# Optimization experiments

Hardware: AMD Instinct MI355X
Metric: run time of the kernel (lower is better)

## Reference

```python
import jax, jax.numpy as jnp
import numpy as np

EMBED_DIM = 1024
NUM_HEADS = 16
HEAD_DIM = EMBED_DIM // NUM_HEADS
EPS = 1e-5


def setup_inputs() -> dict:
    key = jax.random.key(0)
    ks = jax.random.split(key, 7)
    B, S, D = 4, 2048, EMBED_DIM
    s = 1.0 / np.sqrt(D)
    return {
        "x": jax.random.normal(ks[0], (B, S, D), dtype=jnp.float32),
        "W_qkv": jax.random.uniform(ks[1], (D, 3 * D), jnp.float32, -s, s),
        "b_qkv": jax.random.uniform(ks[2], (3 * D,), jnp.float32, -s, s),
        "W_out": jax.random.uniform(ks[3], (D, D), jnp.float32, -s, s),
        "b_out": jax.random.uniform(ks[4], (D,), jnp.float32, -s, s),
        "gamma": jnp.ones((D,), jnp.float32),
        "beta": jnp.zeros((D,), jnp.float32),
    }


def _layer_norm(y, gamma, beta):
    mu = jnp.mean(y, axis=-1, keepdims=True)
    var = jnp.mean(jnp.square(y - mu), axis=-1, keepdims=True)
    return (y - mu) * jax.lax.rsqrt(var + EPS) * gamma + beta


def reference(x, W_qkv, b_qkv, W_out, b_out, gamma, beta):
    B, S, D = x.shape
    H, Hd = NUM_HEADS, HEAD_DIM
    qkv = x @ W_qkv + b_qkv                       # [B,S,3D]
    q, k, v = jnp.split(qkv, 3, axis=-1)
    q = q.reshape(B, S, H, Hd).transpose(0, 2, 1, 3)  # [B,H,S,Hd]
    k = k.reshape(B, S, H, Hd).transpose(0, 2, 1, 3)
    v = v.reshape(B, S, H, Hd).transpose(0, 2, 1, 3)
    scale = 1.0 / np.sqrt(Hd)
    scores = jnp.einsum("bhsd,bhtd->bhst", q, k) * scale  # [B,H,S,S]
    attn = jax.nn.softmax(scores, axis=-1)
    ctx = jnp.einsum("bhst,bhtd->bhsd", attn, v)  # [B,H,S,Hd]
    ctx = ctx.transpose(0, 2, 1, 3).reshape(B, S, D)
    out = ctx @ W_out + b_out
    return _layer_norm(out + x, gamma, beta)
```

## Files before the change

### kernel.cpp

```cpp
#include <hip/hip_runtime.h>
#include <stdint.h>
#include <stddef.h>


#define SEQ    2048
#define DMODEL 1024
#define NHEAD  16
#define HDIM   64

typedef __attribute__((ext_vector_type(4))) float f32x4;
typedef __attribute__((ext_vector_type(16))) float f32x16;
typedef __attribute__((ext_vector_type(8))) short bf16x8;
typedef __attribute__((ext_vector_type(2))) unsigned uint2v;

static __device__ __forceinline__ unsigned short f2b(float f) {
  union { float f; unsigned u; } c; c.f = f;
  unsigned r = c.u + 0x7FFFu + ((c.u >> 16) & 1u);
  return (unsigned short)(r >> 16);
}
static __device__ __forceinline__ unsigned pkbf(float lo, float hi_) {
  unsigned r;
  asm("v_cvt_pk_bf16_f32 %0, %1, %2" : "=v"(r) : "v"(lo), "v"(hi_));
  return r;
}
static __device__ __forceinline__ float exp2v(float x) {
  return __builtin_amdgcn_exp2f(x);
}
static __device__ __forceinline__ uint2v swap32(unsigned a, unsigned b) {
  return __builtin_amdgcn_permlane32_swap(a, b, false, false);
}
static __device__ __forceinline__ float xchg_sum(float v) {
  union { float f; unsigned u; } c; c.f = v;
  uint2v p = swap32(c.u, c.u);
  union { unsigned u; float f; } x, y; x.u = p[0]; y.u = p[1];
  return x.f + y.f;
}
static __device__ __forceinline__ void gl_lds16(const void* g, void* l) {
  __builtin_amdgcn_global_load_lds((const __attribute__((address_space(1))) void*)g,
                                   (__attribute__((address_space(3))) void*)l, 16, 0, 0);
}
static __device__ __forceinline__ int swz(int row, int col) {
  return (row * 64 + col) ^ ((row & 7) << 3);
}

__global__ __launch_bounds__(256) void k_prep(const float* __restrict__ Wqkv,
                                              const float* __restrict__ Wout,
                                              const float* __restrict__ X,
                                              unsigned short* __restrict__ wqkvT,
                                              unsigned short* __restrict__ woutT,
                                              unsigned short* __restrict__ Xb) {
  __shared__ unsigned short tile[32][33];
  const int bid = blockIdx.x;
  const int t = threadIdx.x;
  if (bid < 4096) {
    const float* in; unsigned short* out; int C, bx, by;
    if (bid < 3072) { in = Wqkv; out = wqkvT; C = 3072; bx = bid % 96; by = bid / 96; }
    else { int b2 = bid - 3072; in = Wout; out = woutT; C = 1024; bx = b2 & 31; by = b2 >> 5; }
    const int R = 1024;
    const int c0 = bx * 32, r0 = by * 32;
    const int tx = t & 31, ty = t >> 5;
#pragma unroll
    for (int j = 0; j < 4; j++) {
      int rr = ty + j * 8;
      tile[rr][tx] = f2b(in[(size_t)(r0 + rr) * C + c0 + tx]);
    }
    __syncthreads();
#pragma unroll
    for (int j = 0; j < 4; j++) {
      int rr = ty + j * 8;
      out[(size_t)(c0 + rr) * R + r0 + tx] = tile[tx][rr];
    }
  } else {
    const size_t i = ((size_t)(bid - 4096) * 256 + t) * 8;
    f32x4 a = *(const f32x4*)&X[i];
    f32x4 b = *(const f32x4*)&X[i + 4];
    bf16x8 o;
    o[0] = (short)f2b(a[0]); o[1] = (short)f2b(a[1]);
    o[2] = (short)f2b(a[2]); o[3] = (short)f2b(a[3]);
    o[4] = (short)f2b(b[0]); o[5] = (short)f2b(b[1]);
    o[6] = (short)f2b(b[2]); o[7] = (short)f2b(b[3]);
    *(bf16x8*)&Xb[i] = o;
  }
}

__global__ __launch_bounds__(256) void k_gemm_qkv(const unsigned short* __restrict__ X,
                                                  const unsigned short* __restrict__ WT,
                                                  const float* __restrict__ bias,
                                                  unsigned short* __restrict__ qb,
                                                  unsigned short* __restrict__ kb,
                                                  unsigned short* __restrict__ vt) {
  __shared__ __align__(16) unsigned short As[128 * 32];
  __shared__ __align__(16) unsigned short Bs[128 * 32];
  const int t = threadIdx.x;
  const int w = t >> 6, l = t & 63, g = l >> 4, r = l & 15;
  const int wr = w >> 1, wc = w & 1;
  const int bm = blockIdx.x * 128;
  const int bn = blockIdx.y * 128;

  f32x4 acc[4][4];
#pragma unroll
  for (int a = 0; a < 4; a++)
#pragma unroll
    for (int b = 0; b < 4; b++) acc[a][b] = f32x4{0.f, 0.f, 0.f, 0.f};

  for (int k0 = 0; k0 < DMODEL; k0 += 32) {
    __syncthreads();
#pragma unroll
    for (int j = 0; j < 2; j++) {
      int idx = t + j * 256;
      int row = idx >> 2, kc = idx & 3;
      gl_lds16(X + (size_t)(bm + row) * DMODEL + k0 + kc * 8, (char*)As + idx * 16);
      gl_lds16(WT + (size_t)(bn + row) * DMODEL + k0 + kc * 8, (char*)Bs + idx * 16);
    }
    __syncthreads();
    bf16x8 af[4], bf[4];
#pragma unroll
    for (int mf = 0; mf < 4; mf++)
      af[mf] = *(const bf16x8*)&As[(wr * 64 + mf * 16 + r) * 32 + g * 8];
#pragma unroll
    for (int nf = 0; nf < 4; nf++)
      bf[nf] = *(const bf16x8*)&Bs[(wc * 64 + nf * 16 + r) * 32 + g * 8];
#pragma unroll
    for (int mf = 0; mf < 4; mf++)
#pragma unroll
      for (int nf = 0; nf < 4; nf++)
        acc[mf][nf] = __builtin_amdgcn_mfma_f32_16x16x32_bf16(af[mf], bf[nf], acc[mf][nf], 0, 0, 0);
  }

  if (blockIdx.y >= 16) {
    __syncthreads();
    const int bi = bm >> 11, sbase = bm & 2047;
    const int h  = ((bn - 2048) >> 6) + wc;
    const int bh = bi * NHEAD + h;
    unsigned short* Ls = (w < 2) ? (As + w * 2048) : (Bs + (w - 2) * 2048);
#pragma unroll
    for (int p = 0; p < 2; p++) {
#pragma unroll
      for (int nfp = 0; nfp < 2; nfp++)
#pragma unroll
        for (int mf = 0; mf < 4; mf++)
#pragma unroll
          for (int i = 0; i < 4; i++) {
            const int nf = 2 * p + nfp;
            const int dd = nfp * 16 + r;
            const int ss = mf * 16 + g * 4 + i;
            float v = acc[mf][nf][i] + bias[bn + wc * 64 + nf * 16 + r];
            Ls[dd * 64 + (((ss >> 3) ^ (dd & 7)) * 8) + (ss & 7)] = f2b(v);
          }
#pragma unroll
      for (int j = 0; j < 4; j++) {
        const int dd = l >> 1;
        const int ch = (l & 1) * 4 + j;
        bf16x8 ov = *(const bf16x8*)&Ls[dd * 64 + ((ch ^ (dd & 7)) * 8)];
        *(bf16x8*)&vt[((size_t)bh * HDIM + 32 * p + dd) * SEQ + sbase + wr * 64 + ch * 8] = ov;
      }
    }
  } else {
#pragma unroll
    for (int mf = 0; mf < 4; mf++)
#pragma unroll
      for (int nf = 0; nf < 4; nf++)
#pragma unroll
        for (int i = 0; i < 4; i++) {
          int m = bm + wr * 64 + mf * 16 + g * 4 + i;
          int n = bn + wc * 64 + nf * 16 + r;
          float v = acc[mf][nf][i] + bias[n];
          int part = n >> 10, rem = n & 1023, h = rem >> 6, d = rem & 63;
          int bi = m >> 11, s = m & 2047;
          int bh = bi * NHEAD + h;
          if (part == 0)      qb[((size_t)bh * SEQ + s) * HDIM + d] = f2b(v * 0.18033688f);
          else                kb[((size_t)bh * SEQ + s) * HDIM + d] = f2b(v);
        }
  }
}

__global__ __launch_bounds__(512) void k_attn(const unsigned short* __restrict__ qb,
                                              const unsigned short* __restrict__ kb,
                                              const unsigned short* __restrict__ vt,
                                              unsigned short* __restrict__ ctx) {
  __shared__ __align__(16) unsigned short S[16384];
  unsigned short* K0 = S;
  unsigned short* K1 = S + 4096;
  unsigned short* V0 = S + 8192;
  unsigned short* V1 = S + 12288;
  const int t = threadIdx.x;
  const int w = t >> 6, l = t & 63;
  const int ql = l & 31, hi = l >> 5;
  const int bid = blockIdx.x;
  const int xcd = bid & 7;
  const int j_  = bid >> 3;
  const int bh  = xcd * 8 + (j_ >> 3);
  const int q0  = (j_ & 7) * 256;
  const size_t qoff = ((size_t)bh * SEQ + q0) * HDIM;

#pragma unroll
  for (int j = 0; j < 4; j++) {
    int idx = t + j * 512;
    int row = idx >> 3, s = idx & 7;
    gl_lds16(qb + qoff + (size_t)row * 64 + (s ^ (row & 7)) * 8, (char*)S + idx * 16);
  }
  asm volatile("s_waitcnt vmcnt(0)" ::: "memory");
  __builtin_amdgcn_sched_barrier(0);
  __builtin_amdgcn_s_barrier();

  bf16x8 qf[4];
#pragma unroll
  for (int ds = 0; ds < 4; ds++)
    qf[ds] = *(const bf16x8*)&S[swz(w * 32 + ql, ds * 16 + hi * 8)];
  asm volatile("s_waitcnt lgkmcnt(0)" ::: "memory");
  __builtin_amdgcn_sched_barrier(0);
  __builtin_amdgcn_s_barrier();

  {
    int row = t >> 3, s = t & 7;
    gl_lds16(kb + ((size_t)bh * SEQ + row) * HDIM + (s ^ (row & 7)) * 8, (char*)K0 + t * 16);
    gl_lds16(vt + ((size_t)bh * HDIM + row) * SEQ + (s ^ (row & 7)) * 8, (char*)V0 + t * 16);
  }

  f32x16 acc_o[2];
  float l_run = 0.f;
#pragma unroll
  for (int db = 0; db < 2; db++)
#pragma unroll
    for (int i = 0; i < 16; i++) acc_o[db][i] = 0.f;

  for (int it = 0; it < SEQ / 64; ++it) {
    const int b = it & 1;
    if (it + 1 < SEQ / 64) {
      const int kt = (it + 1) * 64;
      unsigned short* Kd = b ? K0 : K1;
      unsigned short* Vd = b ? V0 : V1;
      {
        int row = t >> 3, s = t & 7;
        gl_lds16(kb + ((size_t)bh * SEQ + kt + row) * HDIM + (s ^ (row & 7)) * 8,
                 (char*)Kd + t * 16);
        gl_lds16(vt + ((size_t)bh * HDIM + row) * SEQ + kt + (s ^ (row & 7)) * 8,
                 (char*)Vd + t * 16);
      }
      asm volatile("s_waitcnt vmcnt(2)" ::: "memory");
    } else {
      asm volatile("s_waitcnt vmcnt(0)" ::: "memory");
    }
    __builtin_amdgcn_sched_barrier(0);
    __builtin_amdgcn_s_barrier();

    const unsigned short* Kb = b ? K1 : K0;
    const unsigned short* Vb = b ? V1 : V0;

    bf16x8 kf[2][4];
#pragma unroll
    for (int kb2 = 0; kb2 < 2; kb2++)
#pragma unroll
      for (int ds = 0; ds < 4; ds++)
        kf[kb2][ds] = *(const bf16x8*)&Kb[swz(kb2 * 32 + ql, ds * 16 + hi * 8)];

    f32x16 accs[2];
#pragma unroll
    for (int kb2 = 0; kb2 < 2; kb2++)
#pragma unroll
      for (int i = 0; i < 16; i++) accs[kb2][i] = 0.f;
    __builtin_amdgcn_s_setprio(1);
#pragma unroll
    for (int ds = 0; ds < 4; ds++)
#pragma unroll
      for (int kb2 = 0; kb2 < 2; kb2++)
        accs[kb2] = __builtin_amdgcn_mfma_f32_32x32x16_bf16(kf[kb2][ds], qf[ds], accs[kb2], 0, 0, 0);
    __builtin_amdgcn_s_setprio(0);

#pragma unroll
    for (int kb2 = 0; kb2 < 2; kb2++)
#pragma unroll
      for (int i = 0; i < 16; i++) accs[kb2][i] = exp2v(accs[kb2][i]);
    float s8[8];
#pragma unroll
    for (int i = 0; i < 8; i++)
      s8[i] = (accs[0][i] + accs[0][i + 8]) + (accs[1][i] + accs[1][i + 8]);
    float sum = ((s8[0] + s8[1]) + (s8[2] + s8[3])) + ((s8[4] + s8[5]) + (s8[6] + s8[7]));
    sum = xchg_sum(sum);
    l_run += sum;

    bf16x8 pa[4];
#pragma unroll
    for (int ks = 0; ks < 4; ks++) {
      const int kb2 = ks >> 1, rb = (ks & 1) * 8;
      unsigned wA0 = pkbf(accs[kb2][rb + 0], accs[kb2][rb + 1]);
      unsigned wA1 = pkbf(accs[kb2][rb + 2], accs[kb2][rb + 3]);
      unsigned wB0 = pkbf(accs[kb2][rb + 4], accs[kb2][rb + 5]);
      unsigned wB1 = pkbf(accs[kb2][rb + 6], accs[kb2][rb + 7]);
      uint2v s0 = swap32(wB0, wA0);
      uint2v s1 = swap32(wB1, wA1);
      union { bf16x8 v; unsigned u[4]; } fr;
      fr.u[0] = s0[1]; fr.u[1] = s1[1]; fr.u[2] = s0[0]; fr.u[3] = s1[0];
      pa[ks] = fr.v;
    }

    bf16x8 vf[2][4];
#pragma unroll
    for (int db = 0; db < 2; db++)
#pragma unroll
      for (int ks = 0; ks < 4; ks++)
        vf[db][ks] = *(const bf16x8*)&Vb[swz(db * 32 + ql, ks * 16 + hi * 8)];

    __builtin_amdgcn_s_setprio(1);
#pragma unroll
    for (int ks = 0; ks < 4; ks++)
#pragma unroll
      for (int db = 0; db < 2; db++)
        acc_o[db] = __builtin_amdgcn_mfma_f32_32x32x16_bf16(vf[db][ks], pa[ks], acc_o[db], 0, 0, 0);
    __builtin_amdgcn_s_setprio(0);

    __builtin_amdgcn_s_barrier();
  }

  const int bi = bh >> 4, h = bh & 15;
  const float rl = 1.f / l_run;
  unsigned short* Ls = S + w * 2048;
#pragma unroll
  for (int db = 0; db < 2; db++)
#pragma unroll
    for (int j = 0; j < 8; j++) {
      const int d0 = db * 32 + (j & 1) * 2 + (j >> 1) * 8 + hi * 4;
      *(unsigned*)&Ls[(ql * 64 + d0) ^ ((ql & 7) << 3)] =
          pkbf(acc_o[db][2 * j] * rl, acc_o[db][2 * j + 1] * rl);
    }
#pragma unroll
  for (int rq = 0; rq < 4; rq++) {
    const int q = rq * 8 + (l >> 3);
    const int c8 = l & 7;
    bf16x8 ov = *(const bf16x8*)&Ls[(q * 64 + c8 * 8) ^ ((q & 7) << 3)];
    *(bf16x8*)&ctx[((size_t)bi * SEQ + q0 + w * 32 + q) * DMODEL + h * 64 + c8 * 8] = ov;
  }
}

__global__ __launch_bounds__(256) void k_gemm_out(const unsigned short* __restrict__ A,
                                                  const unsigned short* __restrict__ WT,
                                                  const float* __restrict__ bias,
                                                  const float* __restrict__ X,
                                                  float* __restrict__ Y) {
  __shared__ __align__(16) unsigned short As[128 * 32];
  __shared__ __align__(16) unsigned short Bs[128 * 32];
  const int t = threadIdx.x;
  const int w = t >> 6, l = t & 63, g = l >> 4, r = l & 15;
  const int wr = w >> 1, wc = w & 1;
  const int bm = blockIdx.x * 128;
  const int bn = blockIdx.y * 128;

  f32x4 acc[4][4];
#pragma unroll
  for (int a = 0; a < 4; a++)
#pragma unroll
    for (int b = 0; b < 4; b++) acc[a][b] = f32x4{0.f, 0.f, 0.f, 0.f};

  for (int k0 = 0; k0 < DMODEL; k0 += 32) {
    __syncthreads();
#pragma unroll
    for (int j = 0; j < 2; j++) {
      int idx = t + j * 256;
      int row = idx >> 2, kc = idx & 3;
      gl_lds16(A + (size_t)(bm + row) * DMODEL + k0 + kc * 8, (char*)As + idx * 16);
      gl_lds16(WT + (size_t)(bn + row) * DMODEL + k0 + kc * 8, (char*)Bs + idx * 16);
    }
    __syncthreads();
    bf16x8 af[4], bf[4];
#pragma unroll
    for (int mf = 0; mf < 4; mf++)
      af[mf] = *(const bf16x8*)&As[(wr * 64 + mf * 16 + r) * 32 + g * 8];
#pragma unroll
    for (int nf = 0; nf < 4; nf++)
      bf[nf] = *(const bf16x8*)&Bs[(wc * 64 + nf * 16 + r) * 32 + g * 8];
#pragma unroll
    for (int mf = 0; mf < 4; mf++)
#pragma unroll
      for (int nf = 0; nf < 4; nf++)
        acc[mf][nf] = __builtin_amdgcn_mfma_f32_16x16x32_bf16(af[mf], bf[nf], acc[mf][nf], 0, 0, 0);
  }

#pragma unroll
  for (int mf = 0; mf < 4; mf++)
#pragma unroll
    for (int nf = 0; nf < 4; nf++)
#pragma unroll
      for (int i = 0; i < 4; i++) {
        int m = bm + wr * 64 + mf * 16 + g * 4 + i;
        int n = bn + wc * 64 + nf * 16 + r;
        float v = acc[mf][nf][i] + bias[n] + X[(size_t)m * DMODEL + n];
        Y[(size_t)m * DMODEL + n] = v;
      }
}

__global__ __launch_bounds__(256) void k_ln(const float* __restrict__ Y,
                                            const float* __restrict__ gamma,
                                            const float* __restrict__ beta,
                                            float* __restrict__ out) {
  const int row = blockIdx.x, t = threadIdx.x;
  const float* y = Y + (size_t)row * DMODEL;
  f32x4 v = *(const f32x4*)&y[t * 4];
  float s = v[0] + v[1] + v[2] + v[3];
  float q = v[0] * v[0] + v[1] * v[1] + v[2] * v[2] + v[3] * v[3];
#pragma unroll
  for (int m = 1; m < 64; m <<= 1) { s += __shfl_xor(s, m); q += __shfl_xor(q, m); }
  __shared__ float ss[4], sq[4];
  const int w = t >> 6, l = t & 63;
  if (l == 0) { ss[w] = s; sq[w] = q; }
  __syncthreads();
  s = ss[0] + ss[1] + ss[2] + ss[3];
  q = sq[0] + sq[1] + sq[2] + sq[3];
  const float mu = s * (1.f / DMODEL);
  const float var = q * (1.f / DMODEL) - mu * mu;
  const float rs = rsqrtf(var + 1e-5f);
  f32x4 o;
#pragma unroll
  for (int j = 0; j < 4; j++)
    o[j] = (v[j] - mu) * rs * gamma[t * 4 + j] + beta[t * 4 + j];
  *(f32x4*)&out[(size_t)row * DMODEL + t * 4] = o;
}

extern "C" void kernel_launch(void* const* d_in, const int* in_sizes, int n_in,
                              void* d_out, int out_size, void* d_ws, size_t ws_size,
                              hipStream_t stream) {
  const float* X     = (const float*)d_in[0];
  const float* Wqkv  = (const float*)d_in[1];
  const float* bqkv  = (const float*)d_in[2];
  const float* Wout  = (const float*)d_in[3];
  const float* bout  = (const float*)d_in[4];
  const float* gamma = (const float*)d_in[5];
  const float* beta  = (const float*)d_in[6];

  char* ws = (char*)d_ws;
  unsigned short* wqkvT = (unsigned short*)(ws);
  unsigned short* woutT = (unsigned short*)(ws + 6291456);
  unsigned short* Xb    = (unsigned short*)(ws + 8388608);
  unsigned short* ctx   = (unsigned short*)(ws + 8388608);
  unsigned short* qb    = (unsigned short*)(ws + 25165824);
  unsigned short* kb    = (unsigned short*)(ws + 41943040);
  unsigned short* vt    = (unsigned short*)(ws + 58720256);
  float*          Yf    = (float*)d_out;

  k_prep<<<dim3(8192, 1, 1), dim3(256, 1, 1), 0, stream>>>(Wqkv, Wout, X, wqkvT, woutT, Xb);
  k_gemm_qkv<<<dim3(64, 24, 1), dim3(256, 1, 1), 0, stream>>>(Xb, wqkvT, bqkv, qb, kb, vt);
  k_attn<<<dim3(512, 1, 1), dim3(512, 1, 1), 0, stream>>>(qb, kb, vt, ctx);
  k_gemm_out<<<dim3(64, 8, 1), dim3(256, 1, 1), 0, stream>>>(ctx, woutT, bout, X, Yf);
  k_ln<<<dim3(8192, 1, 1), dim3(256, 1, 1), 0, stream>>>(Yf, gamma, beta, (float*)d_out);
}
```

Baseline: 204.1 us.

## Double-buffer LDS tiles in QKV and output projection GEMMs

```diff
diff --git a/kernel.cpp b/kernel.cpp
--- a/kernel.cpp
+++ b/kernel.cpp
@@ -89,8 +89,8 @@
                                                   unsigned short* __restrict__ qb,
                                                   unsigned short* __restrict__ kb,
                                                   unsigned short* __restrict__ vt) {
-  __shared__ __align__(16) unsigned short As[128 * 32];
-  __shared__ __align__(16) unsigned short Bs[128 * 32];
+  __shared__ __align__(16) unsigned short As[2][128 * 32];
+  __shared__ __align__(16) unsigned short Bs[2][128 * 32];
   const int t = threadIdx.x;
   const int w = t >> 6, l = t & 63, g = l >> 4, r = l & 15;
   const int wr = w >> 1, wc = w & 1;
@@ -103,36 +103,53 @@
 #pragma unroll
     for (int b = 0; b < 4; b++) acc[a][b] = f32x4{0.f, 0.f, 0.f, 0.f};
 
-  for (int k0 = 0; k0 < DMODEL; k0 += 32) {
-    __syncthreads();
-#pragma unroll
-    for (int j = 0; j < 2; j++) {
-      int idx = t + j * 256;
-      int row = idx >> 2, kc = idx & 3;
-      gl_lds16(X + (size_t)(bm + row) * DMODEL + k0 + kc * 8, (char*)As + idx * 16);
-      gl_lds16(WT + (size_t)(bn + row) * DMODEL + k0 + kc * 8, (char*)Bs + idx * 16);
-    }
-    __syncthreads();
+#pragma unroll
+  for (int j = 0; j < 2; j++) {
+    int idx = t + j * 256;
+    int row = idx >> 2, kc = idx & 3;
+    gl_lds16(X + (size_t)(bm + row) * DMODEL + kc * 8, (char*)As[0] + idx * 16);
+    gl_lds16(WT + (size_t)(bn + row) * DMODEL + kc * 8, (char*)Bs[0] + idx * 16);
+  }
+
+  for (int it = 0; it < DMODEL / 32; ++it) {
+    const int cur = it & 1;
+    if (it + 1 < DMODEL / 32) {
+      const int k0 = (it + 1) * 32;
+#pragma unroll
+      for (int j = 0; j < 2; j++) {
+        int idx = t + j * 256;
+        int row = idx >> 2, kc = idx & 3;
+        gl_lds16(X + (size_t)(bm + row) * DMODEL + k0 + kc * 8, (char*)As[cur ^ 1] + idx * 16);
+        gl_lds16(WT + (size_t)(bn + row) * DMODEL + k0 + kc * 8, (char*)Bs[cur ^ 1] + idx * 16);
+      }
+      asm volatile("s_waitcnt vmcnt(4)" ::: "memory");
+    } else {
+      asm volatile("s_waitcnt vmcnt(0)" ::: "memory");
+    }
+    __builtin_amdgcn_sched_barrier(0);
+    __builtin_amdgcn_s_barrier();
+
     bf16x8 af[4], bf[4];
 #pragma unroll
     for (int mf = 0; mf < 4; mf++)
-      af[mf] = *(const bf16x8*)&As[(wr * 64 + mf * 16 + r) * 32 + g * 8];
+      af[mf] = *(const bf16x8*)&As[cur][(wr * 64 + mf * 16 + r) * 32 + g * 8];
 #pragma unroll
     for (int nf = 0; nf < 4; nf++)
-      bf[nf] = *(const bf16x8*)&Bs[(wc * 64 + nf * 16 + r) * 32 + g * 8];
+      bf[nf] = *(const bf16x8*)&Bs[cur][(wc * 64 + nf * 16 + r) * 32 + g * 8];
 #pragma unroll
     for (int mf = 0; mf < 4; mf++)
 #pragma unroll
       for (int nf = 0; nf < 4; nf++)
         acc[mf][nf] = __builtin_amdgcn_mfma_f32_16x16x32_bf16(af[mf], bf[nf], acc[mf][nf], 0, 0, 0);
+
+    __builtin_amdgcn_s_barrier();
   }
 
   if (blockIdx.y >= 16) {
-    __syncthreads();
     const int bi = bm >> 11, sbase = bm & 2047;
     const int h  = ((bn - 2048) >> 6) + wc;
     const int bh = bi * NHEAD + h;
-    unsigned short* Ls = (w < 2) ? (As + w * 2048) : (Bs + (w - 2) * 2048);
+    unsigned short* Ls = (unsigned short*)As + w * 2048;
 #pragma unroll
     for (int p = 0; p < 2; p++) {
 #pragma unroll
@@ -337,8 +354,8 @@
                                                   const float* __restrict__ bias,
                                                   const float* __restrict__ X,
                                                   float* __restrict__ Y) {
-  __shared__ __align__(16) unsigned short As[128 * 32];
-  __shared__ __align__(16) unsigned short Bs[128 * 32];
+  __shared__ __align__(16) unsigned short As[2][128 * 32];
+  __shared__ __align__(16) unsigned short Bs[2][128 * 32];
   const int t = threadIdx.x;
   const int w = t >> 6, l = t & 63, g = l >> 4, r = l & 15;
   const int wr = w >> 1, wc = w & 1;
@@ -351,28 +368,46 @@
 #pragma unroll
     for (int b = 0; b < 4; b++) acc[a][b] = f32x4{0.f, 0.f, 0.f, 0.f};
 
-  for (int k0 = 0; k0 < DMODEL; k0 += 32) {
-    __syncthreads();
-#pragma unroll
-    for (int j = 0; j < 2; j++) {
-      int idx = t + j * 256;
-      int row = idx >> 2, kc = idx & 3;
-      gl_lds16(A + (size_t)(bm + row) * DMODEL + k0 + kc * 8, (char*)As + idx * 16);
-      gl_lds16(WT + (size_t)(bn + row) * DMODEL + k0 + kc * 8, (char*)Bs + idx * 16);
-    }
-    __syncthreads();
+#pragma unroll
+  for (int j = 0; j < 2; j++) {
+    int idx = t + j * 256;
+    int row = idx >> 2, kc = idx & 3;
+    gl_lds16(A + (size_t)(bm + row) * DMODEL + kc * 8, (char*)As[0] + idx * 16);
+    gl_lds16(WT + (size_t)(bn + row) * DMODEL + kc * 8, (char*)Bs[0] + idx * 16);
+  }
+
+  for (int it = 0; it < DMODEL / 32; ++it) {
+    const int cur = it & 1;
+    if (it + 1 < DMODEL / 32) {
+      const int k0 = (it + 1) * 32;
+#pragma unroll
+      for (int j = 0; j < 2; j++) {
+        int idx = t + j * 256;
+        int row = idx >> 2, kc = idx & 3;
+        gl_lds16(A + (size_t)(bm + row) * DMODEL + k0 + kc * 8, (char*)As[cur ^ 1] + idx * 16);
+        gl_lds16(WT + (size_t)(bn + row) * DMODEL + k0 + kc * 8, (char*)Bs[cur ^ 1] + idx * 16);
+      }
+      asm volatile("s_waitcnt vmcnt(4)" ::: "memory");
+    } else {
+      asm volatile("s_waitcnt vmcnt(0)" ::: "memory");
+    }
+    __builtin_amdgcn_sched_barrier(0);
+    __builtin_amdgcn_s_barrier();
+
     bf16x8 af[4], bf[4];
 #pragma unroll
     for (int mf = 0; mf < 4; mf++)
-      af[mf] = *(const bf16x8*)&As[(wr * 64 + mf * 16 + r) * 32 + g * 8];
+      af[mf] = *(const bf16x8*)&As[cur][(wr * 64 + mf * 16 + r) * 32 + g * 8];
 #pragma unroll
     for (int nf = 0; nf < 4; nf++)
-      bf[nf] = *(const bf16x8*)&Bs[(wc * 64 + nf * 16 + r) * 32 + g * 8];
+      bf[nf] = *(const bf16x8*)&Bs[cur][(wc * 64 + nf * 16 + r) * 32 + g * 8];
 #pragma unroll
     for (int mf = 0; mf < 4; mf++)
 #pragma unroll
       for (int nf = 0; nf < 4; nf++)
         acc[mf][nf] = __builtin_amdgcn_mfma_f32_16x16x32_bf16(af[mf], bf[nf], acc[mf][nf], 0, 0, 0);
+
+    __builtin_amdgcn_s_barrier();
   }
 
 #pragma unroll
```

Measured after the change: 215.9 us. +5.8%, slower.
